# Kernel optimization log

Hardware: AMD Instinct MI355X
Metric: run time of the kernel (lower is better)

Reference implementation:

```python
import jax, jax.numpy as jnp
import numpy as np

B, N, H, HS = 8, 96, 8, 32
NS = H * HS  # 256, also ES
EPS = 1e-5


def _linear(x, w, b):
    return x @ w + b  # w: [in, out]


def _ln(x, g, b):
    m = jnp.mean(x, axis=-1, keepdims=True)
    v = jnp.var(x, axis=-1, keepdims=True)
    return (x - m) * jax.lax.rsqrt(v + EPS) * g + b


def _sep_n(x):  # [B,N,NS] -> [B,H,N,HS]
    b, n, _ = x.shape
    return x.reshape(b, n, H, HS).transpose(0, 2, 1, 3)


def _sep_e(x):  # [B,N,N,ES] -> [B,H,N,N,HS]
    b, n, _, _ = x.shape
    return x.reshape(b, n, n, H, HS).transpose(0, 3, 1, 2, 4)


def setup_inputs() -> dict:
    key = jax.random.key(0)
    ks = jax.random.split(key, 32)
    s = 1.0 / np.sqrt(NS)
    d = {
        "node_tensors": jax.random.normal(ks[0], (B, N, NS), jnp.float32),
        "edge_tensors": jax.random.normal(ks[1], (B, N, N, NS), jnp.float32),
    }
    names = ["Wn", "We", "Wn1", "Wn2", "Wee"]
    for i, nm in enumerate(names):
        d[nm + "_w"] = jax.random.uniform(ks[2 + 2 * i], (3, NS, NS), jnp.float32, -s, s)
        d[nm + "_b"] = jax.random.uniform(ks[3 + 2 * i], (3, NS), jnp.float32, -s, s)
    for i, nm in enumerate(["NL1", "NL2", "EL1", "EL2"]):
        d[nm + "_w"] = jax.random.uniform(ks[12 + 2 * i], (NS, NS), jnp.float32, -s, s)
        d[nm + "_b"] = jax.random.uniform(ks[13 + 2 * i], (NS,), jnp.float32, -s, s)
    d["NLN1_g"] = jnp.ones((NS,), jnp.float32)
    d["NLN1_b"] = jnp.zeros((NS,), jnp.float32)
    d["ELN1_g"] = jnp.ones((NS,), jnp.float32)
    d["ELN1_b"] = jnp.zeros((NS,), jnp.float32)
    return d


def _forward(node_tensors, edge_tensors, Wn_w, Wn_b, We_w, We_b, Wn1_w, Wn1_b,
             Wn2_w, Wn2_b, Wee_w, Wee_b, NL1_w, NL1_b, NL2_w, NL2_b,
             EL1_w, EL1_b, EL2_w, EL2_b, NLN1_g, NLN1_b, ELN1_g, ELN1_b):
    scale = 1.0 / jnp.sqrt(jnp.float32(HS))
    b = node_tensors.shape[0]

    # --- node attention ---
    eQ = _sep_e(_linear(edge_tensors, We_w[0], We_b[0]))
    eK = _sep_e(_linear(edge_tensors, We_w[1], We_b[1]))
    eV = _sep_e(_linear(edge_tensors, We_w[2], We_b[2]))
    nQ = _sep_n(_linear(node_tensors, Wn_w[0], Wn_b[0]))
    nK = _sep_n(_linear(node_tensors, Wn_w[1], Wn_b[1]))
    nV = _sep_n(_linear(node_tensors, Wn_w[2], Wn_b[2]))

    Q = eQ + nQ[:, :, :, None, :]          # [B,H,N,N,HS]
    K = eK + nK[:, :, None, :, :]
    scores = jnp.einsum('bhijc,bhijc->bhij', Q, K) * scale
    attn = jax.nn.softmax(scores, axis=-1)
    V = eV + nV[:, :, None, :, :]
    new_nodes = jnp.einsum('bhij,bhijc->bhic', attn, V)   # [B,H,N,HS]
    attw = new_nodes.transpose(0, 2, 1, 3).reshape(b, N, NS)

    res = _linear(jax.nn.relu(_linear(attw, NL1_w, NL1_b)), NL2_w, NL2_b)
    node_out = _ln(node_tensors + res, NLN1_g, NLN1_b)

    # --- edge update ---
    n1Q = _sep_n(_linear(node_out, Wn1_w[0], Wn1_b[0]))
    n1K = _sep_n(_linear(node_out, Wn1_w[1], Wn1_b[1]))
    n1V = _sep_n(_linear(node_out, Wn1_w[2], Wn1_b[2]))
    n2Q = _sep_n(_linear(node_out, Wn2_w[0], Wn2_b[0]))
    n2K = _sep_n(_linear(node_out, Wn2_w[1], Wn2_b[1]))
    n2V = _sep_n(_linear(node_out, Wn2_w[2], Wn2_b[2]))
    eQe = _sep_e(_linear(edge_tensors, Wee_w[0], Wee_b[0]))
    eKe = _sep_e(_linear(edge_tensors, Wee_w[1], Wee_b[1]))
    eVe = _sep_e(_linear(edge_tensors, Wee_w[2], Wee_b[2]))

    Qe = eQe + n1Q[:, :, :, None, :] + n2Q[:, :, None, :, :]
    Ke = eKe + n1K[:, :, :, None, :] + n2K[:, :, None, :, :]
    se = jnp.einsum('bhijc,bhijc->bhij', Qe, Ke) * scale
    attn_e = jax.nn.silu(se)                               # [B,H,N,N]
    Ve = eVe + n1V[:, :, :, None, :] + n2V[:, :, None, :, :]
    new_edges = attn_e[..., None] * Ve                     # [B,H,N,N,HS]
    attw_e = new_edges.transpose(0, 2, 3, 1, 4).reshape(b, N, N, NS)

    res_e = _linear(jax.nn.relu(_linear(attw_e, EL1_w, EL1_b)), EL2_w, EL2_b)
    edge_out = _ln(edge_tensors + res_e, ELN1_g, ELN1_b)
    return node_out, edge_out


def reference(node_tensors, edge_tensors, Wn_w, Wn_b, We_w, We_b, Wn1_w, Wn1_b,
              Wn2_w, Wn2_b, Wee_w, Wee_b, NL1_w, NL1_b, NL2_w, NL2_b,
              EL1_w, EL1_b, EL2_w, EL2_b, NLN1_g, NLN1_b, ELN1_g, ELN1_b):
    return _forward(node_tensors, edge_tensors, Wn_w, Wn_b, We_w, We_b,
                    Wn1_w, Wn1_b, Wn2_w, Wn2_b, Wee_w, Wee_b, NL1_w, NL1_b,
                    NL2_w, NL2_b, EL1_w, EL1_b, EL2_w, EL2_b,
                    NLN1_g, NLN1_b, ELN1_g, ELN1_b)
```

## Files before the change

kernel.cpp:

```cpp
#include <hip/hip_runtime.h>


#define DI __device__ __forceinline__

typedef float f32x4 __attribute__((ext_vector_type(4)));
typedef short bf16x8 __attribute__((ext_vector_type(8)));

DI unsigned short f2bf(float f) {
  union { float f; unsigned u; } v; v.f = f;
  return (unsigned short)((v.u + 0x7FFFu + ((v.u >> 16) & 1u)) >> 16);
}
DI float bf2f(unsigned short h) {
  union { unsigned u; float f; } v; v.u = ((unsigned)h) << 16;
  return v.f;
}

#define LDE 264
#define SCALE 0.17677669529663687f

#define MFMA(A, B, C) __builtin_amdgcn_mfma_f32_16x16x32_bf16((A), (B), (C), 0, 0, 0)

__global__ __launch_bounds__(256)
void prep_and_qkv(const float* __restrict__ We_w, const float* __restrict__ Wee_w,
                  const float* __restrict__ EL1_w, const float* __restrict__ EL2_w,
                  unsigned short* __restrict__ fb,
                  const float* __restrict__ node, const float* __restrict__ Ww,
                  const float* __restrict__ Wb, float* __restrict__ nQ,
                  float* __restrict__ nK, float* __restrict__ nV)
{
  __shared__ float Wl[32 * 256];
  const int t = threadIdx.x;
  if (blockIdx.x < 64) {
    const int blk = blockIdx.x, kt = blk & 7, ms = blk >> 3;
    const float* src; unsigned short* dst; int NT, ntbase;
    if (ms < 3)       { src = We_w  + ms * 65536;       dst = fb;          NT = 48; ntbase = ms * 16; }
    else if (ms < 6)  { src = Wee_w + (ms - 3) * 65536; dst = fb + 196608; NT = 48; ntbase = (ms - 3) * 16; }
    else if (ms == 6) { src = EL1_w;                    dst = fb + 393216; NT = 16; ntbase = 0; }
    else              { src = EL2_w;                    dst = fb + 458752; NT = 16; ntbase = 0; }
    for (int u = t; u < 32 * 64; u += 256) {
      const int r = u >> 6, c4 = (u & 63) << 2;
      *(float4*)(Wl + r * 256 + c4) = *(const float4*)(src + (kt * 32 + r) * 256 + c4);
    }
    __syncthreads();
    for (int u = t; u < 16 * 64; u += 256) {
      const int ntl = u >> 6, l = u & 63;
      const int kb = (l >> 4) << 3, c = ntl * 16 + (l & 15);
      unsigned short tmp[8];
      #pragma unroll
      for (int i = 0; i < 8; ++i) tmp[i] = f2bf(Wl[(kb + i) * 256 + c]);
      const int nt = ntbase + ntl;
      *(uint4*)(dst + ((size_t)(kt * NT + nt) * 64 + l) * 8) = *(const uint4*)tmp;
    }
  } else {
    float (*x)[256] = (float(*)[256])Wl;
    const int r0 = (blockIdx.x - 64) * 4;
    #pragma unroll
    for (int rr = 0; rr < 4; ++rr) x[rr][t] = node[(r0 + rr) * 256 + t];
    __syncthreads();
    float a0[4], a1[4], a2[4];
    #pragma unroll
    for (int rr = 0; rr < 4; ++rr) { a0[rr] = Wb[t]; a1[rr] = Wb[256 + t]; a2[rr] = Wb[512 + t]; }
    for (int k = 0; k < 256; ++k) {
      const float w0 = Ww[k * 256 + t], w1 = Ww[65536 + k * 256 + t], w2 = Ww[131072 + k * 256 + t];
      #pragma unroll
      for (int rr = 0; rr < 4; ++rr) {
        const float xv = x[rr][k];
        a0[rr] += xv * w0; a1[rr] += xv * w1; a2[rr] += xv * w2;
      }
    }
    const int h = t >> 5, c = t & 31;
    #pragma unroll
    for (int rr = 0; rr < 4; ++rr) {
      const int row = r0 + rr, b = row / 96, j = row - b * 96;
      const int oi = ((b * 8 + h) * 96 + j) * 32 + c;
      nQ[oi] = a0[rr]; nK[oi] = a1[rr]; nV[oi] = a2[rr];
    }
  }
}

__global__ __launch_bounds__(512, 2)
void node_attn(const float* __restrict__ edge, const float* __restrict__ We_b,
               const unsigned short* __restrict__ WeF,
               const float* __restrict__ nQ, const float* __restrict__ nK,
               const float* __restrict__ nV, float* __restrict__ attw)
{
  __shared__ unsigned short Elds[96 * LDE];
  __shared__ float sc[768];
  __shared__ float nQp[256];
  __shared__ float bias[768];

  const int tid = threadIdx.x, lane = tid & 63, wid = tid >> 6;
  const int b = blockIdx.x & 7, i = blockIdx.x >> 3;
  const size_t bi = (size_t)(b * 96 + i);

  if (tid < 256) nQp[tid] = nQ[((b * 8 + (tid >> 5)) * 96 + i) * 32 + (tid & 31)];
  for (int u = tid; u < 768; u += 512) bias[u] = We_b[u];

  const float* Erow = edge + bi * 24576;
  for (int u = tid; u < 96 * 64; u += 512) {
    const int j = u >> 6, g = u & 63;
    const float4 v = *(const float4*)(Erow + j * 256 + g * 4);
    const unsigned lo = (unsigned)f2bf(v.x) | ((unsigned)f2bf(v.y) << 16);
    const unsigned hi = (unsigned)f2bf(v.z) | ((unsigned)f2bf(v.w) << 16);
    *(uint2*)(Elds + j * LDE + g * 4) = make_uint2(lo, hi);
  }
  __syncthreads();

  {
    const int h = wid;
    const unsigned short* wq0 = WeF + ((2 * h) * 64 + lane) * 8;
    const unsigned short* wq1 = WeF + ((2 * h + 1) * 64 + lane) * 8;
    const unsigned short* wk0 = WeF + ((16 + 2 * h) * 64 + lane) * 8;
    const unsigned short* wk1 = WeF + ((17 + 2 * h) * 64 + lane) * 8;
    const int c0 = h * 32 + (lane & 15), c1 = c0 + 16;
    const float qb0 = bias[c0] + nQp[c0], qb1 = bias[c1] + nQp[c1];
    const float kb0 = bias[256 + c0], kb1 = bias[256 + c1];
    for (int half = 0; half < 3; ++half) {
      const f32x4 z = {0.f, 0.f, 0.f, 0.f};
      f32x4 aq0[2] = {z, z}, aq1[2] = {z, z}, ak0[2] = {z, z}, ak1[2] = {z, z};
      for (int kt = 0; kt < 8; ++kt) {
        const bf16x8 b0 = *(const bf16x8*)(wq0 + kt * 24576);
        const bf16x8 b1 = *(const bf16x8*)(wq1 + kt * 24576);
        const bf16x8 b2 = *(const bf16x8*)(wk0 + kt * 24576);
        const bf16x8 b3 = *(const bf16x8*)(wk1 + kt * 24576);
        #pragma unroll
        for (int m = 0; m < 2; ++m) {
          const int mt = half * 2 + m;
          const bf16x8 afr = *(const bf16x8*)(Elds + (mt * 16 + (lane & 15)) * LDE
                                              + ((lane >> 4) << 3) + kt * 32);
          aq0[m] = MFMA(afr, b0, aq0[m]);
          aq1[m] = MFMA(afr, b1, aq1[m]);
          ak0[m] = MFMA(afr, b2, ak0[m]);
          ak1[m] = MFMA(afr, b3, ak1[m]);
        }
      }
      #pragma unroll
      for (int m = 0; m < 2; ++m) {
        const int mt = half * 2 + m;
        float prod[4];
        #pragma unroll
        for (int r = 0; r < 4; ++r) {
          const int j = mt * 16 + ((lane >> 4) << 2) + r;
          const int g = ((b * 8 + h) * 96 + j) * 32;
          const float k0v = ak0[m][r] + kb0 + nK[g + (lane & 15)];
          const float k1v = ak1[m][r] + kb1 + nK[g + 16 + (lane & 15)];
          prod[r] = (aq0[m][r] + qb0) * k0v + (aq1[m][r] + qb1) * k1v;
        }
        #pragma unroll
        for (int mm = 1; mm < 16; mm <<= 1) {
          #pragma unroll
          for (int r = 0; r < 4; ++r) prod[r] += __shfl_xor(prod[r], mm, 64);
        }
        if ((lane & 15) == 0) {
          #pragma unroll
          for (int r = 0; r < 4; ++r)
            sc[h * 96 + mt * 16 + ((lane >> 4) << 2) + r] = prod[r];
        }
      }
    }
  }

  const f32x4 z = {0.f, 0.f, 0.f, 0.f};
  f32x4 accB[6][2] = {{z, z}, {z, z}, {z, z}, {z, z}, {z, z}, {z, z}};
  {
    const unsigned short* wb0 = WeF + ((32 + wid) * 64 + lane) * 8;
    const unsigned short* wb1 = WeF + ((40 + wid) * 64 + lane) * 8;
    for (int kt = 0; kt < 8; ++kt) {
      const bf16x8 b0 = *(const bf16x8*)(wb0 + kt * 24576);
      const bf16x8 b1 = *(const bf16x8*)(wb1 + kt * 24576);
      #pragma unroll
      for (int mt = 0; mt < 6; ++mt) {
        const bf16x8 afr = *(const bf16x8*)(Elds + (mt * 16 + (lane & 15)) * LDE
                                            + ((lane >> 4) << 3) + kt * 32);
        accB[mt][0] = MFMA(afr, b0, accB[mt][0]);
        accB[mt][1] = MFMA(afr, b1, accB[mt][1]);
      }
    }
  }
  __syncthreads();

  {
    const int h = wid;
    const float s0 = sc[h * 96 + lane] * SCALE;
    const float s1 = (lane < 32) ? sc[h * 96 + 64 + lane] * SCALE : -1e30f;
    float mx = fmaxf(s0, s1);
    #pragma unroll
    for (int m = 1; m < 64; m <<= 1) mx = fmaxf(mx, __shfl_xor(mx, m, 64));
    const float e0 = __expf(s0 - mx);
    const float e1 = (lane < 32) ? __expf(s1 - mx) : 0.f;
    float sm = e0 + e1;
    #pragma unroll
    for (int m = 1; m < 64; m <<= 1) sm += __shfl_xor(sm, m, 64);
    const float inv = 1.f / sm;
    sc[h * 96 + lane] = e0 * inv;
    if (lane < 32) sc[h * 96 + 64 + lane] = e1 * inv;
  }
  __syncthreads();

  {
    const int col0 = wid * 16 + (lane & 15), col1 = col0 + 128;
    const int h0 = col0 >> 5, cc0 = col0 & 31;
    const int h1 = col1 >> 5, cc1 = col1 & 31;
    const float base0 = bias[512 + col0], base1 = bias[512 + col1];
    float nn[2] = {0.f, 0.f};
    #pragma unroll
    for (int mt = 0; mt < 6; ++mt) {
      #pragma unroll
      for (int r = 0; r < 4; ++r) {
        const int j = mt * 16 + ((lane >> 4) << 2) + r;
        const float v0 = accB[mt][0][r] + base0 + nV[((b * 8 + h0) * 96 + j) * 32 + cc0];
        const float v1 = accB[mt][1][r] + base1 + nV[((b * 8 + h1) * 96 + j) * 32 + cc1];
        nn[0] += sc[h0 * 96 + j] * v0;
        nn[1] += sc[h1 * 96 + j] * v1;
      }
    }
    #pragma unroll
    for (int s = 0; s < 2; ++s) {
      nn[s] += __shfl_xor(nn[s], 16, 64);
      nn[s] += __shfl_xor(nn[s], 32, 64);
    }
    if (lane < 16) {
      attw[bi * 256 + wid * 16 + lane] = nn[0];
      attw[bi * 256 + (wid + 8) * 16 + lane] = nn[1];
    }
  }
}

__global__ __launch_bounds__(256)
void node_ffn_ln(const float* __restrict__ attw, const float* __restrict__ node,
                 const float* __restrict__ W1, const float* __restrict__ B1,
                 const float* __restrict__ W2, const float* __restrict__ B2,
                 const float* __restrict__ g, const float* __restrict__ be,
                 float* __restrict__ node_out)
{
  __shared__ float xa[8][256];
  __shared__ float h1[8][256];
  __shared__ float xr[8][256];
  const int t = threadIdx.x, r0 = blockIdx.x * 8;
  #pragma unroll
  for (int rr = 0; rr < 8; ++rr) xa[rr][t] = attw[(r0 + rr) * 256 + t];
  __syncthreads();
  float acc[8];
  #pragma unroll
  for (int rr = 0; rr < 8; ++rr) acc[rr] = B1[t];
  for (int k = 0; k < 256; ++k) {
    const float w = W1[k * 256 + t];
    #pragma unroll
    for (int rr = 0; rr < 8; ++rr) acc[rr] += xa[rr][k] * w;
  }
  #pragma unroll
  for (int rr = 0; rr < 8; ++rr) h1[rr][t] = fmaxf(acc[rr], 0.f);
  __syncthreads();
  #pragma unroll
  for (int rr = 0; rr < 8; ++rr) acc[rr] = B2[t];
  for (int k = 0; k < 256; ++k) {
    const float w = W2[k * 256 + t];
    #pragma unroll
    for (int rr = 0; rr < 8; ++rr) acc[rr] += h1[rr][k] * w;
  }
  #pragma unroll
  for (int rr = 0; rr < 8; ++rr) xr[rr][t] = node[(r0 + rr) * 256 + t] + acc[rr];
  __syncthreads();
  const int wid = t >> 6, lane = t & 63;
  const float4 gv = *(const float4*)(g + (lane << 2));
  const float4 bv = *(const float4*)(be + (lane << 2));
  for (int rr = wid * 2; rr < wid * 2 + 2; ++rr) {
    const float4 xv = *(const float4*)(&xr[rr][lane << 2]);
    float s = xv.x + xv.y + xv.z + xv.w;
    float sq = xv.x * xv.x + xv.y * xv.y + xv.z * xv.z + xv.w * xv.w;
    #pragma unroll
    for (int m = 1; m < 64; m <<= 1) { s += __shfl_xor(s, m, 64); sq += __shfl_xor(sq, m, 64); }
    const float mean = s * (1.f / 256.f);
    const float rs = rsqrtf(sq * (1.f / 256.f) - mean * mean + 1e-5f);
    float4 o;
    o.x = (xv.x - mean) * rs * gv.x + bv.x;
    o.y = (xv.y - mean) * rs * gv.y + bv.y;
    o.z = (xv.z - mean) * rs * gv.z + bv.z;
    o.w = (xv.w - mean) * rs * gv.w + bv.w;
    *(float4*)(node_out + (r0 + rr) * 256 + (lane << 2)) = o;
  }
}

__global__ __launch_bounds__(256)
void node_proj6(const float* __restrict__ nodeo,
                const float* __restrict__ W1, const float* __restrict__ B1,
                const float* __restrict__ W2, const float* __restrict__ B2,
                float* __restrict__ n1Q, float* __restrict__ n1K, float* __restrict__ n1V,
                float* __restrict__ n2Q, float* __restrict__ n2K, float* __restrict__ n2V)
{
  __shared__ float x[4][256];
  const int t = threadIdx.x, r0 = blockIdx.x * 4;
  #pragma unroll
  for (int rr = 0; rr < 4; ++rr) x[rr][t] = nodeo[(r0 + rr) * 256 + t];
  __syncthreads();
  float a[6][4];
  #pragma unroll
  for (int rr = 0; rr < 4; ++rr) {
    a[0][rr] = B1[t]; a[1][rr] = B1[256 + t]; a[2][rr] = B1[512 + t];
    a[3][rr] = B2[t]; a[4][rr] = B2[256 + t]; a[5][rr] = B2[512 + t];
  }
  for (int k = 0; k < 256; ++k) {
    const float w0 = W1[k * 256 + t], w1 = W1[65536 + k * 256 + t], w2 = W1[131072 + k * 256 + t];
    const float w3 = W2[k * 256 + t], w4 = W2[65536 + k * 256 + t], w5 = W2[131072 + k * 256 + t];
    #pragma unroll
    for (int rr = 0; rr < 4; ++rr) {
      const float xv = x[rr][k];
      a[0][rr] += xv * w0; a[1][rr] += xv * w1; a[2][rr] += xv * w2;
      a[3][rr] += xv * w3; a[4][rr] += xv * w4; a[5][rr] += xv * w5;
    }
  }
  const int h = t >> 5, c = t & 31;
  #pragma unroll
  for (int rr = 0; rr < 4; ++rr) {
    const int row = r0 + rr, b = row / 96, j = row - b * 96;
    const int oi = ((b * 8 + h) * 96 + j) * 32 + c;
    n1Q[oi] = a[0][rr]; n1K[oi] = a[1][rr]; n1V[oi] = a[2][rr];
    n2Q[oi] = a[3][rr]; n2K[oi] = a[4][rr]; n2V[oi] = a[5][rr];
  }
}

__global__ __launch_bounds__(512, 2)
void edge_update(const float* __restrict__ edge, const float* __restrict__ Wee_b,
                 const unsigned short* __restrict__ WeeF,
                 const unsigned short* __restrict__ EL1F,
                 const unsigned short* __restrict__ EL2F,
                 const float* __restrict__ EL1_b, const float* __restrict__ EL2_b,
                 const float* __restrict__ n1Q, const float* __restrict__ n1K, const float* __restrict__ n1V,
                 const float* __restrict__ n2Q, const float* __restrict__ n2K, const float* __restrict__ n2V,
                 const float* __restrict__ lng, const float* __restrict__ lnb,
                 float* __restrict__ edge_out)
{
  __shared__ unsigned short Elds[96 * LDE];
  __shared__ float se[768];
  __shared__ float bn1[768];
  __shared__ float b12[512];
  __shared__ float lg[256], lb[256];

  const int tid = threadIdx.x, lane = tid & 63, wid = tid >> 6;
  const int b = blockIdx.x & 7, i = blockIdx.x >> 3;
  const size_t bi = (size_t)(b * 96 + i);

  for (int u = tid; u < 768; u += 512) {
    const int q = u >> 8, cn = u & 255, h = cn >> 5, c = cn & 31;
    const float* s = (q == 0) ? n1Q : (q == 1) ? n1K : n1V;
    bn1[u] = Wee_b[u] + s[((b * 8 + h) * 96 + i) * 32 + c];
  }
  b12[tid] = (tid < 256) ? EL1_b[tid] : EL2_b[tid - 256];
  if (tid < 256) { lg[tid] = lng[tid]; lb[tid] = lnb[tid]; }

  const float* Erow = edge + bi * 24576;
  for (int u = tid; u < 96 * 64; u += 512) {
    const int j = u >> 6, g = u & 63;
    const float4 v = *(const float4*)(Erow + j * 256 + g * 4);
    const unsigned lo = (unsigned)f2bf(v.x) | ((unsigned)f2bf(v.y) << 16);
    const unsigned hi = (unsigned)f2bf(v.z) | ((unsigned)f2bf(v.w) << 16);
    *(uint2*)(Elds + j * LDE + g * 4) = make_uint2(lo, hi);
  }
  __syncthreads();

  {
    const int h = wid;
    const unsigned short* wq0 = WeeF + ((2 * h) * 64 + lane) * 8;
    const unsigned short* wq1 = WeeF + ((2 * h + 1) * 64 + lane) * 8;
    const unsigned short* wk0 = WeeF + ((16 + 2 * h) * 64 + lane) * 8;
    const unsigned short* wk1 = WeeF + ((17 + 2 * h) * 64 + lane) * 8;
    const int c0 = h * 32 + (lane & 15), c1 = c0 + 16;
    const float qb0 = bn1[c0], qb1 = bn1[c1];
    const float kb0 = bn1[256 + c0], kb1 = bn1[256 + c1];
    for (int half = 0; half < 3; ++half) {
      const f32x4 z = {0.f, 0.f, 0.f, 0.f};
      f32x4 aq0[2] = {z, z}, aq1[2] = {z, z}, ak0[2] = {z, z}, ak1[2] = {z, z};
      for (int kt = 0; kt < 8; ++kt) {
        const bf16x8 b0 = *(const bf16x8*)(wq0 + kt * 24576);
        const bf16x8 b1 = *(const bf16x8*)(wq1 + kt * 24576);
        const bf16x8 b2 = *(const bf16x8*)(wk0 + kt * 24576);
        const bf16x8 b3 = *(const bf16x8*)(wk1 + kt * 24576);
        #pragma unroll
        for (int m = 0; m < 2; ++m) {
          const int mt = half * 2 + m;
          const bf16x8 afr = *(const bf16x8*)(Elds + (mt * 16 + (lane & 15)) * LDE
                                              + ((lane >> 4) << 3) + kt * 32);
          aq0[m] = MFMA(afr, b0, aq0[m]);
          aq1[m] = MFMA(afr, b1, aq1[m]);
          ak0[m] = MFMA(afr, b2, ak0[m]);
          ak1[m] = MFMA(afr, b3, ak1[m]);
        }
      }
      #pragma unroll
      for (int m = 0; m < 2; ++m) {
        const int mt = half * 2 + m;
        float prod[4];
        #pragma unroll
        for (int r = 0; r < 4; ++r) {
          const int j = mt * 16 + ((lane >> 4) << 2) + r;
          const int g = ((b * 8 + h) * 96 + j) * 32;
          const float q0v = aq0[m][r] + qb0 + n2Q[g + (lane & 15)];
          const float q1v = aq1[m][r] + qb1 + n2Q[g + 16 + (lane & 15)];
          const float k0v = ak0[m][r] + kb0 + n2K[g + (lane & 15)];
          const float k1v = ak1[m][r] + kb1 + n2K[g + 16 + (lane & 15)];
          prod[r] = q0v * k0v + q1v * k1v;
        }
        #pragma unroll
        for (int mm = 1; mm < 16; mm <<= 1) {
          #pragma unroll
          for (int r = 0; r < 4; ++r) prod[r] += __shfl_xor(prod[r], mm, 64);
        }
        if ((lane & 15) == 0) {
          #pragma unroll
          for (int r = 0; r < 4; ++r) {
            const float d = prod[r] * SCALE;
            se[h * 96 + mt * 16 + ((lane >> 4) << 2) + r] = d / (1.f + __expf(-d));
          }
        }
      }
    }
  }

  const f32x4 z = {0.f, 0.f, 0.f, 0.f};
  f32x4 acc[6][2] = {{z, z}, {z, z}, {z, z}, {z, z}, {z, z}, {z, z}};
  {
    const unsigned short* wb0 = WeeF + ((32 + wid) * 64 + lane) * 8;
    const unsigned short* wb1 = WeeF + ((40 + wid) * 64 + lane) * 8;
    for (int kt = 0; kt < 8; ++kt) {
      const bf16x8 b0 = *(const bf16x8*)(wb0 + kt * 24576);
      const bf16x8 b1 = *(const bf16x8*)(wb1 + kt * 24576);
      #pragma unroll
      for (int mt = 0; mt < 6; ++mt) {
        const bf16x8 afr = *(const bf16x8*)(Elds + (mt * 16 + (lane & 15)) * LDE
                                            + ((lane >> 4) << 3) + kt * 32);
        acc[mt][0] = MFMA(afr, b0, acc[mt][0]);
        acc[mt][1] = MFMA(afr, b1, acc[mt][1]);
      }
    }
  }
  __syncthreads();

  {
    const int col0 = wid * 16 + (lane & 15), col1 = col0 + 128;
    const int h0 = col0 >> 5, cc0 = col0 & 31;
    const int h1 = col1 >> 5, cc1 = col1 & 31;
    const float base0 = bn1[512 + col0], base1 = bn1[512 + col1];
    #pragma unroll
    for (int mt = 0; mt < 6; ++mt) {
      #pragma unroll
      for (int r = 0; r < 4; ++r) {
        const int j = mt * 16 + ((lane >> 4) << 2) + r;
        const float v0 = acc[mt][0][r] + base0 + n2V[((b * 8 + h0) * 96 + j) * 32 + cc0];
        const float v1 = acc[mt][1][r] + base1 + n2V[((b * 8 + h1) * 96 + j) * 32 + cc1];
        Elds[j * LDE + col0] = f2bf(se[h0 * 96 + j] * v0);
        Elds[j * LDE + col1] = f2bf(se[h1 * 96 + j] * v1);
      }
    }
  }
  __syncthreads();

  {
    #pragma unroll
    for (int mt = 0; mt < 6; ++mt) { acc[mt][0] = z; acc[mt][1] = z; }
    const unsigned short* wb0 = EL1F + (wid * 64 + lane) * 8;
    const unsigned short* wb1 = EL1F + ((wid + 8) * 64 + lane) * 8;
    for (int kt = 0; kt < 8; ++kt) {
      const bf16x8 b0 = *(const bf16x8*)(wb0 + kt * 8192);
      const bf16x8 b1 = *(const bf16x8*)(wb1 + kt * 8192);
      #pragma unroll
      for (int mt = 0; mt < 6; ++mt) {
        const bf16x8 afr = *(const bf16x8*)(Elds + (mt * 16 + (lane & 15)) * LDE
                                            + ((lane >> 4) << 3) + kt * 32);
        acc[mt][0] = MFMA(afr, b0, acc[mt][0]);
        acc[mt][1] = MFMA(afr, b1, acc[mt][1]);
      }
    }
    __syncthreads();
    const int col0 = wid * 16 + (lane & 15), col1 = col0 + 128;
    const float bv0 = b12[col0], bv1 = b12[col1];
    #pragma unroll
    for (int mt = 0; mt < 6; ++mt) {
      #pragma unroll
      for (int r = 0; r < 4; ++r) {
        const int j = mt * 16 + ((lane >> 4) << 2) + r;
        Elds[j * LDE + col0] = f2bf(fmaxf(acc[mt][0][r] + bv0, 0.f));
        Elds[j * LDE + col1] = f2bf(fmaxf(acc[mt][1][r] + bv1, 0.f));
      }
    }
  }
  __syncthreads();

  {
    #pragma unroll
    for (int mt = 0; mt < 6; ++mt) { acc[mt][0] = z; acc[mt][1] = z; }
    const unsigned short* wb0 = EL2F + (wid * 64 + lane) * 8;
    const unsigned short* wb1 = EL2F + ((wid + 8) * 64 + lane) * 8;
    for (int kt = 0; kt < 8; ++kt) {
      const bf16x8 b0 = *(const bf16x8*)(wb0 + kt * 8192);
      const bf16x8 b1 = *(const bf16x8*)(wb1 + kt * 8192);
      #pragma unroll
      for (int mt = 0; mt < 6; ++mt) {
        const bf16x8 afr = *(const bf16x8*)(Elds + (mt * 16 + (lane & 15)) * LDE
                                            + ((lane >> 4) << 3) + kt * 32);
        acc[mt][0] = MFMA(afr, b0, acc[mt][0]);
        acc[mt][1] = MFMA(afr, b1, acc[mt][1]);
      }
    }
    const int col0 = wid * 16 + (lane & 15), col1 = col0 + 128;
    const float bv0 = b12[256 + col0], bv1 = b12[256 + col1];
    const float g0 = lg[col0], g1 = lg[col1], be0 = lb[col0], be1 = lb[col1];
    __syncthreads();
    #pragma unroll
    for (int mt = 0; mt < 6; ++mt) {
      #pragma unroll
      for (int r = 0; r < 4; ++r) {
        const int j = mt * 16 + ((lane >> 4) << 2) + r;
        acc[mt][0][r] += bv0 + Erow[j * 256 + col0];
        acc[mt][1][r] += bv1 + Erow[j * 256 + col1];
      }
    }
    #pragma unroll
    for (int mt = 0; mt < 6; ++mt) {
      #pragma unroll
      for (int r = 0; r < 4; ++r) {
        float s = acc[mt][0][r] + acc[mt][1][r];
        float q = acc[mt][0][r] * acc[mt][0][r] + acc[mt][1][r] * acc[mt][1][r];
        #pragma unroll
        for (int m = 1; m < 16; m <<= 1) { s += __shfl_xor(s, m, 64); q += __shfl_xor(q, m, 64); }
        if ((lane & 15) == 0) {
          const int j = mt * 16 + ((lane >> 4) << 2) + r;
          se[wid * 96 + j] = s; bn1[wid * 96 + j] = q;
        }
      }
    }
    __syncthreads();
    if (tid < 96) {
      float s = 0.f, q = 0.f;
      #pragma unroll
      for (int w = 0; w < 8; ++w) { s += se[w * 96 + tid]; q += bn1[w * 96 + tid]; }
      const float mean = s * (1.f / 256.f);
      b12[tid] = mean;
      b12[96 + tid] = rsqrtf(q * (1.f / 256.f) - mean * mean + 1e-5f);
    }
    __syncthreads();
    #pragma unroll
    for (int mt = 0; mt < 6; ++mt) {
      #pragma unroll
      for (int r = 0; r < 4; ++r) {
        const int j = mt * 16 + ((lane >> 4) << 2) + r;
        const float mean = b12[j], rs = b12[96 + j];
        Elds[j * LDE + col0] = f2bf((acc[mt][0][r] - mean) * rs * g0 + be0);
        Elds[j * LDE + col1] = f2bf((acc[mt][1][r] - mean) * rs * g1 + be1);
      }
    }
  }
  __syncthreads();

  float* orow = edge_out + bi * 24576;
  for (int j = wid; j < 96; j += 8) {
    const uint2 pk = *(const uint2*)(Elds + j * LDE + (lane << 2));
    float4 o;
    o.x = bf2f((unsigned short)(pk.x & 0xffff));
    o.y = bf2f((unsigned short)(pk.x >> 16));
    o.z = bf2f((unsigned short)(pk.y & 0xffff));
    o.w = bf2f((unsigned short)(pk.y >> 16));
    *(float4*)(orow + j * 256 + (lane << 2)) = o;
  }
}

extern "C" void kernel_launch(void* const* d_in, const int* in_sizes, int n_in,
                              void* d_out, int out_size, void* d_ws, size_t ws_size,
                              hipStream_t stream)
{
  (void)in_sizes; (void)n_in; (void)out_size; (void)ws_size;

  const float* node   = (const float*)d_in[0];
  const float* edge   = (const float*)d_in[1];
  const float* Wn_w   = (const float*)d_in[2];
  const float* Wn_b   = (const float*)d_in[3];
  const float* We_w   = (const float*)d_in[4];
  const float* We_b   = (const float*)d_in[5];
  const float* Wn1_w  = (const float*)d_in[6];
  const float* Wn1_b  = (const float*)d_in[7];
  const float* Wn2_w  = (const float*)d_in[8];
  const float* Wn2_b  = (const float*)d_in[9];
  const float* Wee_w  = (const float*)d_in[10];
  const float* Wee_b  = (const float*)d_in[11];
  const float* NL1_w  = (const float*)d_in[12];
  const float* NL1_b  = (const float*)d_in[13];
  const float* NL2_w  = (const float*)d_in[14];
  const float* NL2_b  = (const float*)d_in[15];
  const float* EL1_w  = (const float*)d_in[16];
  const float* EL1_b  = (const float*)d_in[17];
  const float* EL2_w  = (const float*)d_in[18];
  const float* EL2_b  = (const float*)d_in[19];
  const float* NLN1_g = (const float*)d_in[20];
  const float* NLN1_b = (const float*)d_in[21];
  const float* ELN1_g = (const float*)d_in[22];
  const float* ELN1_b = (const float*)d_in[23];

  float* out = (float*)d_out;
  float* node_out = out;
  float* edge_out = out + 196608;

  float* wsf = (float*)d_ws;
  float* nQ  = wsf;                float* nK  = wsf + 196608;   float* nV  = wsf + 393216;
  float* n1Q = wsf + 589824;       float* n1K = wsf + 786432;   float* n1V = wsf + 983040;
  float* n2Q = wsf + 1179648;      float* n2K = wsf + 1376256;  float* n2V = wsf + 1572864;
  float* attw = wsf + 1769472;
  unsigned short* fb   = (unsigned short*)(wsf + 1966080);
  unsigned short* WeF  = fb;
  unsigned short* WeeF = fb + 196608;
  unsigned short* EL1F = fb + 393216;
  unsigned short* EL2F = fb + 458752;

  prep_and_qkv<<<256, 256, 0, stream>>>(We_w, Wee_w, EL1_w, EL2_w, fb,
                                        node, Wn_w, Wn_b, nQ, nK, nV);
  node_attn<<<768, 512, 0, stream>>>(edge, We_b, WeF, nQ, nK, nV, attw);
  node_ffn_ln<<<96, 256, 0, stream>>>(attw, node, NL1_w, NL1_b, NL2_w, NL2_b,
                                      NLN1_g, NLN1_b, node_out);
  node_proj6<<<192, 256, 0, stream>>>(node_out, Wn1_w, Wn1_b, Wn2_w, Wn2_b,
                                      n1Q, n1K, n1V, n2Q, n2K, n2V);
  edge_update<<<768, 512, 0, stream>>>(edge, Wee_b, WeeF, EL1F, EL2F,
                                       EL1_b, EL2_b, n1Q, n1K, n1V,
                                       n2Q, n2K, n2V, ELN1_g, ELN1_b, edge_out);
}
```

Measured before the change: 285.4 us.

## Fuse node FFN/LN with node projections, regroup QK tiles, add MFMA priority hints

Merges the node FFN+LayerNorm kernel and the six-way node projection kernel into one kernel with 4 rows per block. The LN output stays in shared memory for the projections, which removes one launch and a global round trip. The QK score loops now run 2 passes of 3 M-tiles instead of 3 passes of 2, and the MFMA loops are wrapped in s_setprio raises. The larger passes need more accumulator registers, which may lower occupancy in the big attention and edge kernels.

After: 271.6 us. 4.8% less time.

```diff
diff --git a/kernel.cpp b/kernel.cpp
--- a/kernel.cpp
+++ b/kernel.cpp
@@ -115,17 +115,18 @@
     const int c0 = h * 32 + (lane & 15), c1 = c0 + 16;
     const float qb0 = bias[c0] + nQp[c0], qb1 = bias[c1] + nQp[c1];
     const float kb0 = bias[256 + c0], kb1 = bias[256 + c1];
-    for (int half = 0; half < 3; ++half) {
+    for (int pass = 0; pass < 2; ++pass) {
       const f32x4 z = {0.f, 0.f, 0.f, 0.f};
-      f32x4 aq0[2] = {z, z}, aq1[2] = {z, z}, ak0[2] = {z, z}, ak1[2] = {z, z};
+      f32x4 aq0[3] = {z, z, z}, aq1[3] = {z, z, z}, ak0[3] = {z, z, z}, ak1[3] = {z, z, z};
+      __builtin_amdgcn_s_setprio(1);
       for (int kt = 0; kt < 8; ++kt) {
         const bf16x8 b0 = *(const bf16x8*)(wq0 + kt * 24576);
         const bf16x8 b1 = *(const bf16x8*)(wq1 + kt * 24576);
         const bf16x8 b2 = *(const bf16x8*)(wk0 + kt * 24576);
         const bf16x8 b3 = *(const bf16x8*)(wk1 + kt * 24576);
         #pragma unroll
-        for (int m = 0; m < 2; ++m) {
-          const int mt = half * 2 + m;
+        for (int m = 0; m < 3; ++m) {
+          const int mt = pass * 3 + m;
           const bf16x8 afr = *(const bf16x8*)(Elds + (mt * 16 + (lane & 15)) * LDE
                                               + ((lane >> 4) << 3) + kt * 32);
           aq0[m] = MFMA(afr, b0, aq0[m]);
@@ -134,9 +135,10 @@
           ak1[m] = MFMA(afr, b3, ak1[m]);
         }
       }
-      #pragma unroll
-      for (int m = 0; m < 2; ++m) {
-        const int mt = half * 2 + m;
+      __builtin_amdgcn_s_setprio(0);
+      #pragma unroll
+      for (int m = 0; m < 3; ++m) {
+        const int mt = pass * 3 + m;
         float prod[4];
         #pragma unroll
         for (int r = 0; r < 4; ++r) {
@@ -165,6 +167,7 @@
   {
     const unsigned short* wb0 = WeF + ((32 + wid) * 64 + lane) * 8;
     const unsigned short* wb1 = WeF + ((40 + wid) * 64 + lane) * 8;
+    __builtin_amdgcn_s_setprio(1);
     for (int kt = 0; kt < 8; ++kt) {
       const bf16x8 b0 = *(const bf16x8*)(wb0 + kt * 24576);
       const bf16x8 b1 = *(const bf16x8*)(wb1 + kt * 24576);
@@ -176,6 +179,7 @@
         accB[mt][1] = MFMA(afr, b1, accB[mt][1]);
       }
     }
+    __builtin_amdgcn_s_setprio(0);
   }
   __syncthreads();
 
@@ -227,45 +231,49 @@
 }
 
 __global__ __launch_bounds__(256)
-void node_ffn_ln(const float* __restrict__ attw, const float* __restrict__ node,
-                 const float* __restrict__ W1, const float* __restrict__ B1,
-                 const float* __restrict__ W2, const float* __restrict__ B2,
-                 const float* __restrict__ g, const float* __restrict__ be,
-                 float* __restrict__ node_out)
+void node_tail(const float* __restrict__ attw, const float* __restrict__ node,
+               const float* __restrict__ W1, const float* __restrict__ B1,
+               const float* __restrict__ W2, const float* __restrict__ B2,
+               const float* __restrict__ g, const float* __restrict__ be,
+               const float* __restrict__ P1w, const float* __restrict__ P1b,
+               const float* __restrict__ P2w, const float* __restrict__ P2b,
+               float* __restrict__ node_out,
+               float* __restrict__ n1Q, float* __restrict__ n1K, float* __restrict__ n1V,
+               float* __restrict__ n2Q, float* __restrict__ n2K, float* __restrict__ n2V)
 {
-  __shared__ float xa[8][256];
-  __shared__ float h1[8][256];
-  __shared__ float xr[8][256];
-  const int t = threadIdx.x, r0 = blockIdx.x * 8;
+  __shared__ float xa[4][256];
+  __shared__ float h1[4][256];
+  __shared__ float xo[4][256];
+  const int t = threadIdx.x, r0 = blockIdx.x * 4;
   #pragma unroll
-  for (int rr = 0; rr < 8; ++rr) xa[rr][t] = attw[(r0 + rr) * 256 + t];
-  __syncthreads();
-  float acc[8];
+  for (int rr = 0; rr < 4; ++rr) xa[rr][t] = attw[(r0 + rr) * 256 + t];
+  __syncthreads();
+  float acc[4];
   #pragma unroll
-  for (int rr = 0; rr < 8; ++rr) acc[rr] = B1[t];
+  for (int rr = 0; rr < 4; ++rr) acc[rr] = B1[t];
   for (int k = 0; k < 256; ++k) {
     const float w = W1[k * 256 + t];
     #pragma unroll
-    for (int rr = 0; rr < 8; ++rr) acc[rr] += xa[rr][k] * w;
+    for (int rr = 0; rr < 4; ++rr) acc[rr] += xa[rr][k] * w;
   }
   #pragma unroll
-  for (int rr = 0; rr < 8; ++rr) h1[rr][t] = fmaxf(acc[rr], 0.f);
+  for (int rr = 0; rr < 4; ++rr) h1[rr][t] = fmaxf(acc[rr], 0.f);
   __syncthreads();
   #pragma unroll
-  for (int rr = 0; rr < 8; ++rr) acc[rr] = B2[t];
+  for (int rr = 0; rr < 4; ++rr) acc[rr] = B2[t];
   for (int k = 0; k < 256; ++k) {
     const float w = W2[k * 256 + t];
     #pragma unroll
-    for (int rr = 0; rr < 8; ++rr) acc[rr] += h1[rr][k] * w;
+    for (int rr = 0; rr < 4; ++rr) acc[rr] += h1[rr][k] * w;
   }
   #pragma unroll
-  for (int rr = 0; rr < 8; ++rr) xr[rr][t] = node[(r0 + rr) * 256 + t] + acc[rr];
-  __syncthreads();
-  const int wid = t >> 6, lane = t & 63;
-  const float4 gv = *(const float4*)(g + (lane << 2));
-  const float4 bv = *(const float4*)(be + (lane << 2));
-  for (int rr = wid * 2; rr < wid * 2 + 2; ++rr) {
-    const float4 xv = *(const float4*)(&xr[rr][lane << 2]);
+  for (int rr = 0; rr < 4; ++rr) xo[rr][t] = node[(r0 + rr) * 256 + t] + acc[rr];
+  __syncthreads();
+  {
+    const int wid = t >> 6, lane = t & 63;
+    const float4 gv = *(const float4*)(g + (lane << 2));
+    const float4 bv = *(const float4*)(be + (lane << 2));
+    const float4 xv = *(const float4*)(&xo[wid][lane << 2]);
     float s = xv.x + xv.y + xv.z + xv.w;
     float sq = xv.x * xv.x + xv.y * xv.y + xv.z * xv.z + xv.w * xv.w;
     #pragma unroll
@@ -277,34 +285,22 @@
     o.y = (xv.y - mean) * rs * gv.y + bv.y;
     o.z = (xv.z - mean) * rs * gv.z + bv.z;
     o.w = (xv.w - mean) * rs * gv.w + bv.w;
-    *(float4*)(node_out + (r0 + rr) * 256 + (lane << 2)) = o;
-  }
-}
-
-__global__ __launch_bounds__(256)
-void node_proj6(const float* __restrict__ nodeo,
-                const float* __restrict__ W1, const float* __restrict__ B1,
-                const float* __restrict__ W2, const float* __restrict__ B2,
-                float* __restrict__ n1Q, float* __restrict__ n1K, float* __restrict__ n1V,
-                float* __restrict__ n2Q, float* __restrict__ n2K, float* __restrict__ n2V)
-{
-  __shared__ float x[4][256];
-  const int t = threadIdx.x, r0 = blockIdx.x * 4;
-  #pragma unroll
-  for (int rr = 0; rr < 4; ++rr) x[rr][t] = nodeo[(r0 + rr) * 256 + t];
+    *(float4*)(&xo[wid][lane << 2]) = o;
+    *(float4*)(node_out + (r0 + wid) * 256 + (lane << 2)) = o;
+  }
   __syncthreads();
   float a[6][4];
   #pragma unroll
   for (int rr = 0; rr < 4; ++rr) {
-    a[0][rr] = B1[t]; a[1][rr] = B1[256 + t]; a[2][rr] = B1[512 + t];
-    a[3][rr] = B2[t]; a[4][rr] = B2[256 + t]; a[5][rr] = B2[512 + t];
+    a[0][rr] = P1b[t]; a[1][rr] = P1b[256 + t]; a[2][rr] = P1b[512 + t];
+    a[3][rr] = P2b[t]; a[4][rr] = P2b[256 + t]; a[5][rr] = P2b[512 + t];
   }
   for (int k = 0; k < 256; ++k) {
-    const float w0 = W1[k * 256 + t], w1 = W1[65536 + k * 256 + t], w2 = W1[131072 + k * 256 + t];
-    const float w3 = W2[k * 256 + t], w4 = W2[65536 + k * 256 + t], w5 = W2[131072 + k * 256 + t];
+    const float w0 = P1w[k * 256 + t], w1 = P1w[65536 + k * 256 + t], w2 = P1w[131072 + k * 256 + t];
+    const float w3 = P2w[k * 256 + t], w4 = P2w[65536 + k * 256 + t], w5 = P2w[131072 + k * 256 + t];
     #pragma unroll
     for (int rr = 0; rr < 4; ++rr) {
-      const float xv = x[rr][k];
+      const float xv = xo[rr][k];
       a[0][rr] += xv * w0; a[1][rr] += xv * w1; a[2][rr] += xv * w2;
       a[3][rr] += xv * w3; a[4][rr] += xv * w4; a[5][rr] += xv * w5;
     }
@@ -367,17 +363,18 @@
     const int c0 = h * 32 + (lane & 15), c1 = c0 + 16;
     const float qb0 = bn1[c0], qb1 = bn1[c1];
     const float kb0 = bn1[256 + c0], kb1 = bn1[256 + c1];
-    for (int half = 0; half < 3; ++half) {
+    for (int pass = 0; pass < 2; ++pass) {
       const f32x4 z = {0.f, 0.f, 0.f, 0.f};
-      f32x4 aq0[2] = {z, z}, aq1[2] = {z, z}, ak0[2] = {z, z}, ak1[2] = {z, z};
+      f32x4 aq0[3] = {z, z, z}, aq1[3] = {z, z, z}, ak0[3] = {z, z, z}, ak1[3] = {z, z, z};
+      __builtin_amdgcn_s_setprio(1);
       for (int kt = 0; kt < 8; ++kt) {
         const bf16x8 b0 = *(const bf16x8*)(wq0 + kt * 24576);
         const bf16x8 b1 = *(const bf16x8*)(wq1 + kt * 24576);
         const bf16x8 b2 = *(const bf16x8*)(wk0 + kt * 24576);
         const bf16x8 b3 = *(const bf16x8*)(wk1 + kt * 24576);
         #pragma unroll
-        for (int m = 0; m < 2; ++m) {
-          const int mt = half * 2 + m;
+        for (int m = 0; m < 3; ++m) {
+          const int mt = pass * 3 + m;
           const bf16x8 afr = *(const bf16x8*)(Elds + (mt * 16 + (lane & 15)) * LDE
                                               + ((lane >> 4) << 3) + kt * 32);
           aq0[m] = MFMA(afr, b0, aq0[m]);
@@ -386,9 +383,10 @@
           ak1[m] = MFMA(afr, b3, ak1[m]);
         }
       }
-      #pragma unroll
-      for (int m = 0; m < 2; ++m) {
-        const int mt = half * 2 + m;
+      __builtin_amdgcn_s_setprio(0);
+      #pragma unroll
+      for (int m = 0; m < 3; ++m) {
+        const int mt = pass * 3 + m;
         float prod[4];
         #pragma unroll
         for (int r = 0; r < 4; ++r) {
@@ -421,6 +419,7 @@
   {
     const unsigned short* wb0 = WeeF + ((32 + wid) * 64 + lane) * 8;
     const unsigned short* wb1 = WeeF + ((40 + wid) * 64 + lane) * 8;
+    __builtin_amdgcn_s_setprio(1);
     for (int kt = 0; kt < 8; ++kt) {
       const bf16x8 b0 = *(const bf16x8*)(wb0 + kt * 24576);
       const bf16x8 b1 = *(const bf16x8*)(wb1 + kt * 24576);
@@ -432,6 +431,7 @@
         acc[mt][1] = MFMA(afr, b1, acc[mt][1]);
       }
     }
+    __builtin_amdgcn_s_setprio(0);
   }
   __syncthreads();
 
@@ -459,6 +459,7 @@
     for (int mt = 0; mt < 6; ++mt) { acc[mt][0] = z; acc[mt][1] = z; }
     const unsigned short* wb0 = EL1F + (wid * 64 + lane) * 8;
     const unsigned short* wb1 = EL1F + ((wid + 8) * 64 + lane) * 8;
+    __builtin_amdgcn_s_setprio(1);
     for (int kt = 0; kt < 8; ++kt) {
       const bf16x8 b0 = *(const bf16x8*)(wb0 + kt * 8192);
       const bf16x8 b1 = *(const bf16x8*)(wb1 + kt * 8192);
@@ -470,6 +471,7 @@
         acc[mt][1] = MFMA(afr, b1, acc[mt][1]);
       }
     }
+    __builtin_amdgcn_s_setprio(0);
     __syncthreads();
     const int col0 = wid * 16 + (lane & 15), col1 = col0 + 128;
     const float bv0 = b12[col0], bv1 = b12[col1];
@@ -490,6 +492,7 @@
     for (int mt = 0; mt < 6; ++mt) { acc[mt][0] = z; acc[mt][1] = z; }
     const unsigned short* wb0 = EL2F + (wid * 64 + lane) * 8;
     const unsigned short* wb1 = EL2F + ((wid + 8) * 64 + lane) * 8;
+    __builtin_amdgcn_s_setprio(1);
     for (int kt = 0; kt < 8; ++kt) {
       const bf16x8 b0 = *(const bf16x8*)(wb0 + kt * 8192);
       const bf16x8 b1 = *(const bf16x8*)(wb1 + kt * 8192);
@@ -501,6 +504,7 @@
         acc[mt][1] = MFMA(afr, b1, acc[mt][1]);
       }
     }
+    __builtin_amdgcn_s_setprio(0);
     const int col0 = wid * 16 + (lane & 15), col1 = col0 + 128;
     const float bv0 = b12[256 + col0], bv1 = b12[256 + col1];
     const float g0 = lg[col0], g1 = lg[col1], be0 = lb[col0], be1 = lb[col1];
@@ -612,10 +616,9 @@
   prep_and_qkv<<<256, 256, 0, stream>>>(We_w, Wee_w, EL1_w, EL2_w, fb,
                                         node, Wn_w, Wn_b, nQ, nK, nV);
   node_attn<<<768, 512, 0, stream>>>(edge, We_b, WeF, nQ, nK, nV, attw);
-  node_ffn_ln<<<96, 256, 0, stream>>>(attw, node, NL1_w, NL1_b, NL2_w, NL2_b,
-                                      NLN1_g, NLN1_b, node_out);
-  node_proj6<<<192, 256, 0, stream>>>(node_out, Wn1_w, Wn1_b, Wn2_w, Wn2_b,
-                                      n1Q, n1K, n1V, n2Q, n2K, n2V);
+  node_tail<<<192, 256, 0, stream>>>(attw, node, NL1_w, NL1_b, NL2_w, NL2_b,
+                                     NLN1_g, NLN1_b, Wn1_w, Wn1_b, Wn2_w, Wn2_b,
+                                     node_out, n1Q, n1K, n1V, n2Q, n2K, n2V);
   edge_update<<<768, 512, 0, stream>>>(edge, Wee_b, WeeF, EL1F, EL2F,
                                        EL1_b, EL2_b, n1Q, n1K, n1V,
                                        n2Q, n2K, n2V, ELN1_g, ELN1_b, edge_out);
```
